# Kernel optimization log

Measured on AMD Instinct MI355X. Metric: run time of the kernel, lower is better.

The kernel has to match this reference:

```python
import jax, jax.numpy as jnp
import numpy as np

L, D, H = 4096, 1024, 16
HEAD_DIM = D // H
SCALE = 1.0 / float(np.sqrt(HEAD_DIM))


def setup_inputs() -> dict:
    key = jax.random.key(0)
    kq, kk, kv = jax.random.split(key, 3)
    Q = jax.random.normal(kq, (L, D), dtype=jnp.float32)
    K = jax.random.normal(kk, (L, D), dtype=jnp.float32)
    V = jax.random.normal(kv, (L, D), dtype=jnp.float32)
    return {"Q": Q, "K": K, "V": V}


def reference(Q, K, V):
    # [L, D] -> [H, L, head_dim]; contiguous head slices of D (matches the
    # original per-head slicing Q[:, h*hd:(h+1)*hd]).
    q = Q.reshape(L, H, HEAD_DIM).transpose(1, 0, 2)
    k = K.reshape(L, H, HEAD_DIM).transpose(1, 0, 2)
    v = V.reshape(L, H, HEAD_DIM).transpose(1, 0, 2)
    # scores: [H, L, L]
    scores = jnp.einsum('hqd,hkd->hqk', q, k) * SCALE
    probs = jax.nn.softmax(scores, axis=-1)
    out = jnp.einsum('hqk,hkd->hqd', probs, v)  # [H, L, head_dim]
    # merge heads back to [L, D]
    return out.transpose(1, 0, 2).reshape(L, D)
```

## Files before the change

### kernel.cpp

```cpp
#include <hip/hip_runtime.h>
#include <hip/hip_bf16.h>

#define SEQ_L 4096
#define DIM_D 1024
#define NHEAD 16
#define HDIM  64
#define QBLK  64
#define KVB   128
#define NTILE (SEQ_L / KVB)
#define QSCALE 0.180336880f
#define NSHIFT -17.3123405f

typedef __attribute__((ext_vector_type(8))) short bf16x8;
typedef __attribute__((ext_vector_type(4))) short bf16x4;
typedef __attribute__((ext_vector_type(4))) float f32x4;

__device__ __forceinline__ short f2bf(float f) {
    union { float f; unsigned u; } x; x.f = f;
    unsigned r = x.u + 0x7fffu + ((x.u >> 16) & 1u);
    return (short)(r >> 16);
}

__device__ __forceinline__ float fast_exp2(float x) {
#if __has_builtin(__builtin_amdgcn_exp2f)
    return __builtin_amdgcn_exp2f(x);
#else
    return exp2f(x);
#endif
}

__device__ __forceinline__ bf16x4 pk4t(float p0, float p1, float p2, float p3) {
#if __has_builtin(__builtin_amdgcn_perm)
    union { float f; unsigned u; } a0, a1, a2, a3;
    a0.f = p0; a1.f = p1; a2.f = p2; a3.f = p3;
    union { unsigned u[2]; bf16x4 v; } cv;
    cv.u[0] = __builtin_amdgcn_perm(a1.u, a0.u, 0x07060302u);
    cv.u[1] = __builtin_amdgcn_perm(a3.u, a2.u, 0x07060302u);
    return cv.v;
#else
    const bf16x4 r = { f2bf(p0), f2bf(p1), f2bf(p2), f2bf(p3) };
    return r;
#endif
}

__device__ __forceinline__ f32x4 mfma16(bf16x4 a, bf16x4 b, f32x4 c) {
#if __has_builtin(__builtin_amdgcn_mfma_f32_16x16x16bf16_1k)
    return __builtin_amdgcn_mfma_f32_16x16x16bf16_1k(a, b, c, 0, 0, 0);
#else
    asm("v_mfma_f32_16x16x16_bf16 %0, %1, %2, %0" : "+v"(c) : "v"(a), "v"(b));
    return c;
#endif
}

__device__ __forceinline__ void gl16(const void* g, void* l) {
    __builtin_amdgcn_global_load_lds(
        (const __attribute__((address_space(1))) unsigned int*)g,
        (__attribute__((address_space(3))) unsigned int*)l, 16, 0, 0);
}

__global__ void cvt_qk(const float* __restrict__ Q, const float* __restrict__ K,
                       short* __restrict__ Qb, short* __restrict__ Kb) {
    const size_t n8 = (size_t)SEQ_L * DIM_D / 8;
    size_t j = (size_t)blockIdx.x * blockDim.x + threadIdx.x;
    const float* src; short* dst; float sc;
    if (j < n8) { src = Q; dst = Qb; sc = QSCALE; }
    else        { src = K; dst = Kb; sc = 1.0f; j -= n8; }
    const float4 a = *(const float4*)(src + j*8);
    const float4 b = *(const float4*)(src + j*8 + 4);
    bf16x8 v;
    v[0]=f2bf(a.x*sc); v[1]=f2bf(a.y*sc); v[2]=f2bf(a.z*sc); v[3]=f2bf(a.w*sc);
    v[4]=f2bf(b.x*sc); v[5]=f2bf(b.y*sc); v[6]=f2bf(b.z*sc); v[7]=f2bf(b.w*sc);
    *(bf16x8*)(dst + j*8) = v;
}

__global__ void cvt_vT(const float* __restrict__ V, short* __restrict__ VT) {
    __shared__ short tile[64][136];
    const int t = threadIdx.x;
    const int kv0 = blockIdx.x * 128;
    const int h = blockIdx.y;
#pragma unroll
    for (int i = 0; i < 8; ++i) {
        const int idx = i*256 + t;
        const int row = idx >> 4, cg = idx & 15;
        const float4 v = *(const float4*)(V + (size_t)(kv0+row)*DIM_D + h*HDIM + cg*4);
        tile[cg*4+0][row] = f2bf(v.x);
        tile[cg*4+1][row] = f2bf(v.y);
        tile[cg*4+2][row] = f2bf(v.z);
        tile[cg*4+3][row] = f2bf(v.w);
    }
    __syncthreads();
#pragma unroll
    for (int i = 0; i < 4; ++i) {
        const int idx = i*256 + t;
        const int d = idx >> 4, cg = idx & 15;
        *(bf16x8*)(VT + ((size_t)h*HDIM + d)*SEQ_L + kv0 + cg*8) = *(const bf16x8*)&tile[d][cg*8];
    }
}

__launch_bounds__(256, 2)
__global__ void attn_split(const short* __restrict__ Qb, const short* __restrict__ Kb,
                           const short* __restrict__ VT, float* __restrict__ Og) {
    __shared__ union {
        struct { short K[2][KVB*64]; short V[2][HDIM*KVB]; } s;
        struct { float Ob0[64*68]; float Ob1[64*68]; float ls[4][64]; } r;
    } u;

    const int t = threadIdx.x;
    const int w = t >> 6, lane = t & 63;
    const int g = lane >> 4, c = lane & 15;
    const int c7 = c & 7;

    const int flat = blockIdx.x;
    const int f2 = (flat & 7) * 128 + (flat >> 3);
    const int h = f2 >> 6, qi = f2 & 63;
    const int qb = qi * QBLK, hc = h * HDIM;

    bf16x8 qa[4][2];
#pragma unroll
    for (int qt = 0; qt < 4; ++qt)
#pragma unroll
        for (int ds = 0; ds < 2; ++ds)
            qa[qt][ds] = *(const bf16x8*)&Qb[(size_t)(qb + qt*16 + c) * DIM_D + hc + ds*32 + g*8];

    f32x4 o[4][4];
    float psum[4];
#pragma unroll
    for (int qt = 0; qt < 4; ++qt) {
        psum[qt] = 0.f;
#pragma unroll
        for (int db = 0; db < 4; ++db) o[qt][db] = (f32x4){0.f,0.f,0.f,0.f};
    }

    int koff[4], vgo[4]; unsigned kdst[4], vdst[4];
#pragma unroll
    for (int i = 0; i < 4; ++i) {
        const int krow = w*32 + i*8 + (lane >> 3);
        koff[i] = krow * DIM_D + (((lane & 7) ^ (krow & 7)) * 8);
        kdst[i] = (unsigned)(w*32 + i*8) * 128;
        const int bb  = 2*i + (lane >> 5);
        const int vkt = bb >> 2, vdb = bb & 3;
        const int lp  = lane & 31;
        vgo[i]  = (vdb*16 + (lp >> 1)) * SEQ_L + w*32 + vkt*16 + (lp & 1)*8;
        vdst[i] = (unsigned)(w*8 + 2*i) * 512;
    }

    const short* Kh  = Kb + hc;
    const short* VTh = VT + (size_t)h * HDIM * SEQ_L;
    const int vslot  = (c*4 + g) * 4;
    const int vwbase = w * 2048;

#pragma unroll
    for (int i = 0; i < 4; ++i) {
        gl16(Kh + koff[i], (char*)u.s.K[0] + kdst[i]);
        gl16(VTh + vgo[i], (char*)u.s.V[0] + vdst[i]);
    }

    for (int tile = 0; tile < NTILE; ++tile) {
        const int cur = tile & 1;
        if (tile + 1 < NTILE) {
            const short* Kt = Kh + (size_t)(tile + 1) * KVB * DIM_D;
            const short* Vt = VTh + (tile + 1) * KVB;
#pragma unroll
            for (int i = 0; i < 4; ++i) {
                gl16(Kt + koff[i], (char*)u.s.K[cur ^ 1] + kdst[i]);
                gl16(Vt + vgo[i], (char*)u.s.V[cur ^ 1] + vdst[i]);
            }
            asm volatile("s_waitcnt vmcnt(8)" ::: "memory");
        } else {
            asm volatile("s_waitcnt vmcnt(0)" ::: "memory");
        }
        __builtin_amdgcn_sched_barrier(0);

        bf16x8 kf[2][2];
#pragma unroll
        for (int ktl = 0; ktl < 2; ++ktl)
#pragma unroll
            for (int ds = 0; ds < 2; ++ds)
                kf[ktl][ds] = *(const bf16x8*)&u.s.K[cur][(w*32 + ktl*16 + c)*64 + (((ds*4 + g) ^ c7) * 8)];

        bf16x4 vv[2][4];
#pragma unroll
        for (int ktl = 0; ktl < 2; ++ktl)
#pragma unroll
            for (int db = 0; db < 4; ++db)
                vv[ktl][db] = *(const bf16x4*)&u.s.V[cur][vwbase + (ktl*4 + db)*256 + vslot];

        __builtin_amdgcn_s_setprio(1);
#pragma unroll
        for (int qt = 0; qt < 4; ++qt) {
            f32x4 a0 = (f32x4){NSHIFT, NSHIFT, NSHIFT, NSHIFT};
            f32x4 a1 = (f32x4){NSHIFT, NSHIFT, NSHIFT, NSHIFT};
            a0 = __builtin_amdgcn_mfma_f32_16x16x32_bf16(kf[0][0], qa[qt][0], a0, 0, 0, 0);
            a0 = __builtin_amdgcn_mfma_f32_16x16x32_bf16(kf[0][1], qa[qt][1], a0, 0, 0, 0);
            a1 = __builtin_amdgcn_mfma_f32_16x16x32_bf16(kf[1][0], qa[qt][0], a1, 0, 0, 0);
            a1 = __builtin_amdgcn_mfma_f32_16x16x32_bf16(kf[1][1], qa[qt][1], a1, 0, 0, 0);

            const float p00 = fast_exp2(a0[0]), p01 = fast_exp2(a0[1]);
            const float p02 = fast_exp2(a0[2]), p03 = fast_exp2(a0[3]);
            const float p10 = fast_exp2(a1[0]), p11 = fast_exp2(a1[1]);
            const float p12 = fast_exp2(a1[2]), p13 = fast_exp2(a1[3]);
            psum[qt] += (p00 + p01) + (p02 + p03) + (p10 + p11) + (p12 + p13);
            const bf16x4 pb0 = pk4t(p00, p01, p02, p03);
            const bf16x4 pb1 = pk4t(p10, p11, p12, p13);

#pragma unroll
            for (int db = 0; db < 4; ++db) {
                o[qt][db] = mfma16(vv[0][db], pb0, o[qt][db]);
                o[qt][db] = mfma16(vv[1][db], pb1, o[qt][db]);
            }
        }
        __builtin_amdgcn_s_setprio(0);
    }

#pragma unroll
    for (int qt = 0; qt < 4; ++qt) {
        psum[qt] += __shfl_xor(psum[qt], 16);
        psum[qt] += __shfl_xor(psum[qt], 32);
    }
    __syncthreads();
    if (lane < 16) {
#pragma unroll
        for (int qt = 0; qt < 4; ++qt) u.r.ls[w][qt*16 + c] = psum[qt];
    }
    if (w == 0) {
#pragma unroll
        for (int qt = 0; qt < 4; ++qt)
#pragma unroll
            for (int db = 0; db < 4; ++db)
                *(f32x4*)&u.r.Ob0[(qt*16 + c)*68 + db*16 + 4*g] = o[qt][db];
    } else if (w == 1) {
#pragma unroll
        for (int qt = 0; qt < 4; ++qt)
#pragma unroll
            for (int db = 0; db < 4; ++db)
                *(f32x4*)&u.r.Ob1[(qt*16 + c)*68 + db*16 + 4*g] = o[qt][db];
    }
    __syncthreads();
    if (w == 2) {
#pragma unroll
        for (int qt = 0; qt < 4; ++qt)
#pragma unroll
            for (int db = 0; db < 4; ++db) {
                f32x4* p = (f32x4*)&u.r.Ob0[(qt*16 + c)*68 + db*16 + 4*g];
                f32x4 s = *p;
#pragma unroll
                for (int r = 0; r < 4; ++r) s[r] += o[qt][db][r];
                *p = s;
            }
    } else if (w == 3) {
#pragma unroll
        for (int qt = 0; qt < 4; ++qt)
#pragma unroll
            for (int db = 0; db < 4; ++db) {
                f32x4* p = (f32x4*)&u.r.Ob1[(qt*16 + c)*68 + db*16 + 4*g];
                f32x4 s = *p;
#pragma unroll
                for (int r = 0; r < 4; ++r) s[r] += o[qt][db][r];
                *p = s;
            }
    }
    __syncthreads();

    {
        const int row = w*16 + (lane >> 2);
        const int cq = lane & 3;
        const float lt = u.r.ls[0][row] + u.r.ls[1][row] + u.r.ls[2][row] + u.r.ls[3][row];
        const float inv = 1.0f / lt;
        float* op = Og + (size_t)(qb + row) * DIM_D + hc + cq*16;
#pragma unroll
        for (int i = 0; i < 4; ++i) {
            float4 v;
            v.x = (u.r.Ob0[row*68 + cq*16 + i*4 + 0] + u.r.Ob1[row*68 + cq*16 + i*4 + 0]) * inv;
            v.y = (u.r.Ob0[row*68 + cq*16 + i*4 + 1] + u.r.Ob1[row*68 + cq*16 + i*4 + 1]) * inv;
            v.z = (u.r.Ob0[row*68 + cq*16 + i*4 + 2] + u.r.Ob1[row*68 + cq*16 + i*4 + 2]) * inv;
            v.w = (u.r.Ob0[row*68 + cq*16 + i*4 + 3] + u.r.Ob1[row*68 + cq*16 + i*4 + 3]) * inv;
            *(float4*)(op + i*4) = v;
        }
    }
}

#define LDKF 72
__global__ void attn_fwd_fallback(const float* __restrict__ Qg, const float* __restrict__ Kg,
                                  const float* __restrict__ Vg, float* __restrict__ Og) {
    __shared__ short Klds[64 * LDKF];
    __shared__ short Vt[HDIM * LDKF];
    __shared__ short Plds[4 * 16 * LDKF];

    const int t = threadIdx.x;
    const int w = t >> 6, lane = t & 63;
    const int g = lane >> 4, c = lane & 15;
    const int qb = blockIdx.x * 64;
    const int h = blockIdx.y, hc = h * HDIM;

    bf16x8 qa[2];
    {
        const int qrow = qb + w * 16 + c;
        const float* qp = Qg + (size_t)qrow * DIM_D + hc + g * 8;
#pragma unroll
        for (int db = 0; db < 2; ++db) {
            bf16x8 a2;
#pragma unroll
            for (int j = 0; j < 8; ++j) a2[j] = f2bf(qp[db * 32 + j] * 0.125f);
            qa[db] = a2;
        }
    }
    float m[4], lsum[4];
    f32x4 o[4];
#pragma unroll
    for (int r = 0; r < 4; ++r) { m[r] = -1e30f; lsum[r] = 0.f; }
#pragma unroll
    for (int db = 0; db < 4; ++db) o[db] = (f32x4){0.f,0.f,0.f,0.f};
    const int tr = t >> 4, tc = t & 15;

    for (int kv0 = 0; kv0 < SEQ_L; kv0 += 64) {
#pragma unroll
        for (int i = 0; i < 4; ++i) {
            const int kv = tr + i * 16;
            const float4 kf4 = *(const float4*)(Kg + (size_t)(kv0 + kv) * DIM_D + hc + tc * 4);
            short4 ks; ks.x = f2bf(kf4.x); ks.y = f2bf(kf4.y); ks.z = f2bf(kf4.z); ks.w = f2bf(kf4.w);
            *(short4*)&Klds[kv * LDKF + tc * 4] = ks;
            const float4 vf4 = *(const float4*)(Vg + (size_t)(kv0 + kv) * DIM_D + hc + tc * 4);
            Vt[(tc*4+0) * LDKF + kv] = f2bf(vf4.x);
            Vt[(tc*4+1) * LDKF + kv] = f2bf(vf4.y);
            Vt[(tc*4+2) * LDKF + kv] = f2bf(vf4.z);
            Vt[(tc*4+3) * LDKF + kv] = f2bf(vf4.w);
        }
        __syncthreads();
        f32x4 acc[4];
#pragma unroll
        for (int kt = 0; kt < 4; ++kt) {
            f32x4 a2 = (f32x4){0.f,0.f,0.f,0.f};
#pragma unroll
            for (int db = 0; db < 2; ++db) {
                bf16x8 kb = *(const bf16x8*)&Klds[(kt*16 + c) * LDKF + db*32 + g*8];
                a2 = __builtin_amdgcn_mfma_f32_16x16x32_bf16(qa[db], kb, a2, 0, 0, 0);
            }
            acc[kt] = a2;
        }
        float tmax[4];
#pragma unroll
        for (int r = 0; r < 4; ++r)
            tmax[r] = fmaxf(fmaxf(acc[0][r], acc[1][r]), fmaxf(acc[2][r], acc[3][r]));
#pragma unroll
        for (int mask = 1; mask < 16; mask <<= 1)
#pragma unroll
            for (int r = 0; r < 4; ++r) tmax[r] = fmaxf(tmax[r], __shfl_xor(tmax[r], mask));
        float alpha[4], ps[4];
#pragma unroll
        for (int r = 0; r < 4; ++r) {
            const float mn = fmaxf(m[r], tmax[r]);
            alpha[r] = __expf(m[r] - mn); m[r] = mn; ps[r] = 0.f;
        }
#pragma unroll
        for (int kt = 0; kt < 4; ++kt)
#pragma unroll
            for (int r = 0; r < 4; ++r) {
                const float p = __expf(acc[kt][r] - m[r]);
                ps[r] += p;
                Plds[(w*16 + g*4 + r) * LDKF + kt*16 + c] = f2bf(p);
            }
#pragma unroll
        for (int mask = 1; mask < 16; mask <<= 1)
#pragma unroll
            for (int r = 0; r < 4; ++r) ps[r] += __shfl_xor(ps[r], mask);
#pragma unroll
        for (int r = 0; r < 4; ++r) lsum[r] = lsum[r] * alpha[r] + ps[r];
#pragma unroll
        for (int db = 0; db < 4; ++db)
#pragma unroll
            for (int r = 0; r < 4; ++r) o[db][r] *= alpha[r];
#pragma unroll
        for (int db = 0; db < 4; ++db)
#pragma unroll
            for (int kb = 0; kb < 2; ++kb) {
                bf16x8 pa = *(const bf16x8*)&Plds[(w*16 + c) * LDKF + kb*32 + g*8];
                bf16x8 vb = *(const bf16x8*)&Vt[(db*16 + c) * LDKF + kb*32 + g*8];
                o[db] = __builtin_amdgcn_mfma_f32_16x16x32_bf16(pa, vb, o[db], 0, 0, 0);
            }
        __syncthreads();
    }
#pragma unroll
    for (int r = 0; r < 4; ++r) {
        const float inv = 1.0f / lsum[r];
        const int qrow = qb + w*16 + g*4 + r;
        float* op = Og + (size_t)qrow * DIM_D + hc;
#pragma unroll
        for (int db = 0; db < 4; ++db) op[db*16 + c] = o[db][r] * inv;
    }
}

extern "C" void kernel_launch(void* const* d_in, const int* in_sizes, int n_in,
                              void* d_out, int out_size, void* d_ws, size_t ws_size,
                              hipStream_t stream) {
    (void)in_sizes; (void)n_in; (void)out_size;
    const float* Q = (const float*)d_in[0];
    const float* K = (const float*)d_in[1];
    const float* V = (const float*)d_in[2];
    float* O = (float*)d_out;

    const size_t n = (size_t)SEQ_L * DIM_D;
    const size_t need = 3 * n * sizeof(short);
    if (ws_size >= need) {
        short* Qb = (short*)d_ws;
        short* Kb = Qb + n;
        short* VT = Qb + 2 * n;
        hipLaunchKernelGGL(cvt_qk, dim3(2 * n / 8 / 256), dim3(256), 0, stream, Q, K, Qb, Kb);
        hipLaunchKernelGGL(cvt_vT, dim3(SEQ_L / 128, NHEAD), dim3(256), 0, stream, V, VT);
        hipLaunchKernelGGL(attn_split, dim3(1024), dim3(256), 0, stream, Qb, Kb, VT, O);
    } else {
        hipLaunchKernelGGL(attn_fwd_fallback, dim3(SEQ_L / 64, NHEAD), dim3(256), 0, stream, Q, K, V, O);
    }
}
```

Before: 114.1 us.

## Process two KV tiles per iteration with register-staged operands and batched prefetch

The KV loop now handles two tiles per iteration. It loads both tiles' K and V fragments from shared memory into registers, then issues global-to-LDS loads for the next two tiles into the same buffers while computing on the registers. The aim is to halve the number of loop-level waits and give each QK^T/exp/PV block twice as much independent MFMA work. The cost is more register pressure, and a full vmcnt(0) wait at the top of each iteration that exposes latency if the prefetch does not finish during compute.

Result: slower. 116.5 us (+2.1%).

```diff
diff --git a/kernel.cpp b/kernel.cpp
--- a/kernel.cpp
+++ b/kernel.cpp
@@ -154,59 +154,92 @@
         gl16(Kh + koff[i], (char*)u.s.K[0] + kdst[i]);
         gl16(VTh + vgo[i], (char*)u.s.V[0] + vdst[i]);
     }
-
-    for (int tile = 0; tile < NTILE; ++tile) {
-        const int cur = tile & 1;
-        if (tile + 1 < NTILE) {
-            const short* Kt = Kh + (size_t)(tile + 1) * KVB * DIM_D;
-            const short* Vt = VTh + (tile + 1) * KVB;
+#pragma unroll
+    for (int i = 0; i < 4; ++i) {
+        gl16(Kh + (size_t)KVB * DIM_D + koff[i], (char*)u.s.K[1] + kdst[i]);
+        gl16(VTh + KVB + vgo[i], (char*)u.s.V[1] + vdst[i]);
+    }
+
+    for (int tp = 0; tp < NTILE; tp += 2) {
+        asm volatile("s_waitcnt vmcnt(0)" ::: "memory");
+        __builtin_amdgcn_sched_barrier(0);
+
+        bf16x8 kfA[2][2], kfB[2][2];
+        bf16x4 vvA[2][4], vvB[2][4];
+#pragma unroll
+        for (int ktl = 0; ktl < 2; ++ktl)
+#pragma unroll
+            for (int ds = 0; ds < 2; ++ds) {
+                const int ko = (w*32 + ktl*16 + c)*64 + (((ds*4 + g) ^ c7) * 8);
+                kfA[ktl][ds] = *(const bf16x8*)&u.s.K[0][ko];
+                kfB[ktl][ds] = *(const bf16x8*)&u.s.K[1][ko];
+            }
+#pragma unroll
+        for (int ktl = 0; ktl < 2; ++ktl)
+#pragma unroll
+            for (int db = 0; db < 4; ++db) {
+                const int vo = vwbase + (ktl*4 + db)*256 + vslot;
+                vvA[ktl][db] = *(const bf16x4*)&u.s.V[0][vo];
+                vvB[ktl][db] = *(const bf16x4*)&u.s.V[1][vo];
+            }
+
+        asm volatile("s_waitcnt lgkmcnt(0)" ::: "memory");
+        __builtin_amdgcn_sched_barrier(0);
+
+        if (tp + 2 < NTILE) {
+            const short* K2 = Kh + (size_t)(tp + 2) * KVB * DIM_D;
+            const short* V2 = VTh + (tp + 2) * KVB;
+            const short* K3 = K2 + (size_t)KVB * DIM_D;
+            const short* V3 = V2 + KVB;
 #pragma unroll
             for (int i = 0; i < 4; ++i) {
-                gl16(Kt + koff[i], (char*)u.s.K[cur ^ 1] + kdst[i]);
-                gl16(Vt + vgo[i], (char*)u.s.V[cur ^ 1] + vdst[i]);
-            }
-            asm volatile("s_waitcnt vmcnt(8)" ::: "memory");
-        } else {
-            asm volatile("s_waitcnt vmcnt(0)" ::: "memory");
-        }
-        __builtin_amdgcn_sched_barrier(0);
-
-        bf16x8 kf[2][2];
-#pragma unroll
-        for (int ktl = 0; ktl < 2; ++ktl)
-#pragma unroll
-            for (int ds = 0; ds < 2; ++ds)
-                kf[ktl][ds] = *(const bf16x8*)&u.s.K[cur][(w*32 + ktl*16 + c)*64 + (((ds*4 + g) ^ c7) * 8)];
-
-        bf16x4 vv[2][4];
-#pragma unroll
-        for (int ktl = 0; ktl < 2; ++ktl)
-#pragma unroll
-            for (int db = 0; db < 4; ++db)
-                vv[ktl][db] = *(const bf16x4*)&u.s.V[cur][vwbase + (ktl*4 + db)*256 + vslot];
+                gl16(K2 + koff[i], (char*)u.s.K[0] + kdst[i]);
+                gl16(V2 + vgo[i], (char*)u.s.V[0] + vdst[i]);
+            }
+#pragma unroll
+            for (int i = 0; i < 4; ++i) {
+                gl16(K3 + koff[i], (char*)u.s.K[1] + kdst[i]);
+                gl16(V3 + vgo[i], (char*)u.s.V[1] + vdst[i]);
+            }
+        }
 
         __builtin_amdgcn_s_setprio(1);
 #pragma unroll
         for (int qt = 0; qt < 4; ++qt) {
             f32x4 a0 = (f32x4){NSHIFT, NSHIFT, NSHIFT, NSHIFT};
             f32x4 a1 = (f32x4){NSHIFT, NSHIFT, NSHIFT, NSHIFT};
-            a0 = __builtin_amdgcn_mfma_f32_16x16x32_bf16(kf[0][0], qa[qt][0], a0, 0, 0, 0);
-            a0 = __builtin_amdgcn_mfma_f32_16x16x32_bf16(kf[0][1], qa[qt][1], a0, 0, 0, 0);
-            a1 = __builtin_amdgcn_mfma_f32_16x16x32_bf16(kf[1][0], qa[qt][0], a1, 0, 0, 0);
-            a1 = __builtin_amdgcn_mfma_f32_16x16x32_bf16(kf[1][1], qa[qt][1], a1, 0, 0, 0);
-
-            const float p00 = fast_exp2(a0[0]), p01 = fast_exp2(a0[1]);
-            const float p02 = fast_exp2(a0[2]), p03 = fast_exp2(a0[3]);
-            const float p10 = fast_exp2(a1[0]), p11 = fast_exp2(a1[1]);
-            const float p12 = fast_exp2(a1[2]), p13 = fast_exp2(a1[3]);
-            psum[qt] += (p00 + p01) + (p02 + p03) + (p10 + p11) + (p12 + p13);
-            const bf16x4 pb0 = pk4t(p00, p01, p02, p03);
-            const bf16x4 pb1 = pk4t(p10, p11, p12, p13);
+            f32x4 b0 = (f32x4){NSHIFT, NSHIFT, NSHIFT, NSHIFT};
+            f32x4 b1 = (f32x4){NSHIFT, NSHIFT, NSHIFT, NSHIFT};
+            a0 = __builtin_amdgcn_mfma_f32_16x16x32_bf16(kfA[0][0], qa[qt][0], a0, 0, 0, 0);
+            a0 = __builtin_amdgcn_mfma_f32_16x16x32_bf16(kfA[0][1], qa[qt][1], a0, 0, 0, 0);
+            a1 = __builtin_amdgcn_mfma_f32_16x16x32_bf16(kfA[1][0], qa[qt][0], a1, 0, 0, 0);
+            a1 = __builtin_amdgcn_mfma_f32_16x16x32_bf16(kfA[1][1], qa[qt][1], a1, 0, 0, 0);
+            b0 = __builtin_amdgcn_mfma_f32_16x16x32_bf16(kfB[0][0], qa[qt][0], b0, 0, 0, 0);
+            b0 = __builtin_amdgcn_mfma_f32_16x16x32_bf16(kfB[0][1], qa[qt][1], b0, 0, 0, 0);
+            b1 = __builtin_amdgcn_mfma_f32_16x16x32_bf16(kfB[1][0], qa[qt][0], b1, 0, 0, 0);
+            b1 = __builtin_amdgcn_mfma_f32_16x16x32_bf16(kfB[1][1], qa[qt][1], b1, 0, 0, 0);
+
+            const float pa0 = fast_exp2(a0[0]), pa1 = fast_exp2(a0[1]);
+            const float pa2 = fast_exp2(a0[2]), pa3 = fast_exp2(a0[3]);
+            const float pa4 = fast_exp2(a1[0]), pa5 = fast_exp2(a1[1]);
+            const float pa6 = fast_exp2(a1[2]), pa7 = fast_exp2(a1[3]);
+            const float pb0f = fast_exp2(b0[0]), pb1f = fast_exp2(b0[1]);
+            const float pb2f = fast_exp2(b0[2]), pb3f = fast_exp2(b0[3]);
+            const float pb4f = fast_exp2(b1[0]), pb5f = fast_exp2(b1[1]);
+            const float pb6f = fast_exp2(b1[2]), pb7f = fast_exp2(b1[3]);
+            psum[qt] += ((pa0 + pa1) + (pa2 + pa3)) + ((pa4 + pa5) + (pa6 + pa7))
+                      + ((pb0f + pb1f) + (pb2f + pb3f)) + ((pb4f + pb5f) + (pb6f + pb7f));
+            const bf16x4 pA0 = pk4t(pa0, pa1, pa2, pa3);
+            const bf16x4 pA1 = pk4t(pa4, pa5, pa6, pa7);
+            const bf16x4 pB0 = pk4t(pb0f, pb1f, pb2f, pb3f);
+            const bf16x4 pB1 = pk4t(pb4f, pb5f, pb6f, pb7f);
 
 #pragma unroll
             for (int db = 0; db < 4; ++db) {
-                o[qt][db] = mfma16(vv[0][db], pb0, o[qt][db]);
-                o[qt][db] = mfma16(vv[1][db], pb1, o[qt][db]);
+                o[qt][db] = mfma16(vvA[0][db], pA0, o[qt][db]);
+                o[qt][db] = mfma16(vvA[1][db], pA1, o[qt][db]);
+                o[qt][db] = mfma16(vvB[0][db], pB0, o[qt][db]);
+                o[qt][db] = mfma16(vvB[1][db], pB1, o[qt][db]);
             }
         }
         __builtin_amdgcn_s_setprio(0);
```
